# Kernel tuning notes

Measured on AMD Instinct MI355X. Metric: run time of the kernel, lower is better.

## Reference

```python
import jax, jax.numpy as jnp
import numpy as np

N, T, D, H = 2048, 4, 64, 4  # nodes, time steps, per-head dim (=dim), heads


def setup_inputs() -> dict:
    key = jax.random.key(0)
    ks = jax.random.split(key, 9)
    x = jax.random.normal(ks[0], (N, T, D), dtype=jnp.float32)
    Wq = jax.random.normal(ks[1], (H * D, D), dtype=jnp.float32) * 0.05
    bq = jnp.zeros((H * D,), dtype=jnp.float32)
    Wk = jax.random.normal(ks[2], (H * D, D), dtype=jnp.float32) * 0.05
    bk = jnp.zeros((H * D,), dtype=jnp.float32)
    Wv = jax.random.normal(ks[3], (H * D, D), dtype=jnp.float32) * 0.05
    bv = jnp.zeros((H * D,), dtype=jnp.float32)
    attention_weights = jax.random.uniform(ks[4], (T, H, N, N), dtype=jnp.float32)
    attention_mask = jax.random.bernoulli(ks[5], 0.1, (T, H, N, N))
    return {"x": x, "Wq": Wq, "bq": bq, "Wk": Wk, "bk": bk, "Wv": Wv, "bv": bv,
            "attention_weights": attention_weights, "attention_mask": attention_mask}


def reference(x, Wq, bq, Wk, bk, Wv, bv, attention_weights, attention_mask):
    n, t, d = x.shape
    h = Wq.shape[0] // d

    def proj(W, b):
        # (N,T,H*D) -> (N,T,H,D) -> (T,H,N,D)
        return (x @ W.T + b).reshape(n, t, h, d).transpose(1, 2, 0, 3)

    q = proj(Wq, bq)
    k = proj(Wk, bk)
    v = proj(Wv, bv)

    scores = jnp.einsum('thnd,thmd->thnm', q, k) / (d ** 0.5)  # (T,H,N,N)

    raw_att = jax.nn.softmax(scores, axis=-1)
    # torch permutes (T,H,N,D)->(H,N,T,D) contiguous then views as (N,T,H*D);
    # reproduce that exact memory reinterpretation.
    out_raw = jnp.einsum('thnm,thmd->thnd', raw_att, v).transpose(1, 2, 0, 3).reshape(n, t, h * d)

    att = scores * attention_weights
    att = jnp.where(attention_mask, -jnp.inf, att)
    att = jax.nn.softmax(att, axis=-1)
    out = jnp.einsum('thnm,thmd->thnd', att, v).transpose(1, 2, 0, 3).reshape(n, t, h * d)

    return (out, out_raw, raw_att[-1, 0, :, :])
```

## Files before the change

kernel.cpp:

```cpp
#include <hip/hip_runtime.h>
#include <hip/hip_bf16.h>

typedef __attribute__((ext_vector_type(8))) short short8;
typedef __attribute__((ext_vector_type(4))) float float4v;
typedef __attribute__((ext_vector_type(4))) int   int4v;

constexpr int NN = 2048;
constexpr int TT = 4;
constexpr int HH = 4;
constexpr int DD = 64;
constexpr int THC = TT * HH;
constexpr int NTILE = NN / 64;

__device__ __forceinline__ float bf2f(unsigned short u) {
    union { unsigned int i; float f; } c; c.i = ((unsigned int)u) << 16; return c.f;
}
__device__ __forceinline__ unsigned short f2bf(float f) {
    union { float f; unsigned int i; } c; c.f = f;
    unsigned int x = c.i;
    x += 0x7FFFu + ((x >> 16) & 1u);
    return (unsigned short)(x >> 16);
}

__device__ __forceinline__ int mask_code_of(const unsigned int* mw) {
    int okInt = 1, okF32 = 1, okB = 1, anyLow = 0;
    for (int i = 0; i < 256; i++) {
        unsigned int w = mw[i];
        if (w > 1u) okInt = 0;
        if (!(w == 0u || w == 0x3F800000u)) okF32 = 0;
        unsigned int lo = w & 0xFFFFu, hi = w >> 16;
        if (!((lo == 0u || lo == 0x3F80u) && (hi == 0u || hi == 0x3F80u))) okB = 0;
        if (lo == 0x3F80u) anyLow = 1;
    }
    if (okInt) return 1;
    if (okF32 && !anyLow) return 2;
    if (okB) return 3;
    return 0;
}

__device__ __forceinline__ void load_mask_raw(const void* p, size_t idx, int code,
                                              int4v mr[4]) {
    if (code == 1) {
        const int4v* mp = (const int4v*)((const int*)p + idx);
        #pragma unroll
        for (int q = 0; q < 4; q++) mr[q] = mp[q];
    } else if (code == 2) {
        const int4v* mp = (const int4v*)((const float*)p + idx);
        #pragma unroll
        for (int q = 0; q < 4; q++) mr[q] = mp[q];
    } else if (code == 3) {
        const int4v* mp = (const int4v*)((const unsigned short*)p + idx);
        mr[0] = mp[0]; mr[1] = mp[1];
    } else {
        mr[0] = *(const int4v*)((const unsigned char*)p + idx);
    }
}
__device__ __forceinline__ unsigned decode_pm(const int4v mr[4], int code) {
    unsigned pm = 0u;
    if (code == 1) {
        #pragma unroll
        for (int q = 0; q < 4; q++)
            #pragma unroll
            for (int e = 0; e < 4; e++)
                if (mr[q][e] != 0) pm |= 1u << (q * 4 + e);
    } else if (code == 2) {
        #pragma unroll
        for (int q = 0; q < 4; q++)
            #pragma unroll
            for (int e = 0; e < 4; e++)
                if ((((unsigned)mr[q][e]) << 1) != 0u) pm |= 1u << (q * 4 + e);
    } else if (code == 3) {
        #pragma unroll
        for (int q = 0; q < 2; q++)
            #pragma unroll
            for (int e = 0; e < 4; e++) {
                unsigned w = (unsigned)mr[q][e];
                if (w & 0xFFFFu) pm |= 1u << (q * 8 + e * 2);
                if (w >> 16)     pm |= 1u << (q * 8 + e * 2 + 1);
            }
    } else {
        #pragma unroll
        for (int q = 0; q < 4; q++) {
            unsigned w = (unsigned)mr[0][q];
            #pragma unroll
            for (int b = 0; b < 4; b++)
                if ((w >> (8 * b)) & 0xFFu) pm |= 1u << (q * 4 + b);
        }
    }
    return pm;
}

constexpr int PROJ_ROWS = 8;
__global__ __launch_bounds__(256) void proj_b16v_kernel(
    const float* __restrict__ x,
    const float* __restrict__ Wq, const float* __restrict__ bq,
    const float* __restrict__ Wk, const float* __restrict__ bk,
    const float* __restrict__ Wv, const float* __restrict__ bv,
    unsigned short* __restrict__ q16, unsigned short* __restrict__ k16,
    unsigned short* __restrict__ v16)
{
    __shared__ float xl[PROJ_ROWS][64];
    const int tid = threadIdx.x;
    const int r0 = blockIdx.x * PROJ_ROWS;
    for (int i = tid; i < PROJ_ROWS * 64; i += 256)
        xl[i >> 6][i & 63] = x[(size_t)r0 * 64 + i];
    __syncthreads();

    const int c = tid;
    const int hh = c >> 6, dd = c & 63;
    const float* Ws[3] = { Wq, Wk, Wv };
    const float* bs[3] = { bq, bk, bv };
    unsigned short* os[3] = { q16, k16, v16 };

    #pragma unroll
    for (int m = 0; m < 3; m++) {
        float4v wr4[16];
        #pragma unroll
        for (int i = 0; i < 16; i++)
            wr4[i] = *(const float4v*)&Ws[m][(size_t)c * 64 + i * 4];
        const float bias = bs[m][c];
        #pragma unroll
        for (int rr = 0; rr < PROJ_ROWS; rr++) {
            float a = bias;
            #pragma unroll
            for (int i = 0; i < 16; i++) {
                a = fmaf(wr4[i][0], xl[rr][4*i+0], a);
                a = fmaf(wr4[i][1], xl[rr][4*i+1], a);
                a = fmaf(wr4[i][2], xl[rr][4*i+2], a);
                a = fmaf(wr4[i][3], xl[rr][4*i+3], a);
            }
            if (m == 0) a *= 0.125f;
            const int r = r0 + rr;
            const int n = r >> 2, t = r & 3;
            const int th = t * HH + hh;
            os[m][((size_t)th * NN + n) * DD + dd] = f2bf(a);
        }
    }
}

__global__ __launch_bounds__(128, 2) void attn_mfma3_kernel(
    const unsigned short* __restrict__ q16, const unsigned short* __restrict__ k16,
    const unsigned short* __restrict__ v16,
    const float* __restrict__ watt, const void* __restrict__ maskp,
    float* __restrict__ out, float* __restrict__ out_raw)
{
    const int code = mask_code_of((const unsigned int*)maskp);
    const int tid  = threadIdx.x;
    const int wv   = tid >> 6;
    const int lane = tid & 63;
    const int g    = lane >> 4;
    const int j0   = lane & 15;
    const int lr   = lane >> 2;
    const int lc   = lane & 3;

    const int gid = blockIdx.x;
    const int th  = ((gid & 7) << 1) | ((gid >> 3) & 1);
    const int bx  = gid >> 4;
    const int t = th >> 2, h = th & 3;
    const int row0 = bx * 32 + wv * 16;

    const unsigned short* Qb = q16 + (size_t)th * NN * DD;
    const unsigned short* Kb = k16 + (size_t)th * NN * DD;
    const unsigned short* Vb = v16 + (size_t)th * NN * DD;

    __shared__ unsigned short Kl[64][80];
    __shared__ unsigned short Vt[64][80];
    __shared__ float          Sl[2][16][68];
    __shared__ unsigned short Pl[2][16][80];

    short8 aq0, aq1;
    {
        const unsigned short* qp = Qb + (size_t)(row0 + j0) * DD + g * 8;
        aq0 = *(const short8*)qp;
        aq1 = *(const short8*)(qp + 32);
    }

    float m_r = -1e30f, l_r = 0.f, m_w = -1e30f, l_w = 0.f;
    float4v o_r[4], o_w[4];
    #pragma unroll
    for (int ns = 0; ns < 4; ns++) {
        o_r[ns] = (float4v){0.f, 0.f, 0.f, 0.f};
        o_w[ns] = (float4v){0.f, 0.f, 0.f, 0.f};
    }

    const size_t mrow = ((size_t)th * NN + row0 + lr) * NN;

    const int kr = tid >> 1;
    const int kc = (tid & 1) << 5;
    const unsigned short* Kp = Kb + (size_t)kr * DD + kc;
    const unsigned short* Vp = Vb + (size_t)kr * DD + kc;

    short8  kreg[4], vreg[4];
    float4v wcur[4], wnxt[4];
    int4v   mnxt[4];
    unsigned pm;

    #pragma unroll
    for (int u = 0; u < 4; u++) {
        kreg[u] = ((const short8*)Kp)[u];
        vreg[u] = ((const short8*)Vp)[u];
    }
    {
        const float* wp = watt + mrow + lc * 16;
        #pragma unroll
        for (int q = 0; q < 4; q++) wcur[q] = *(const float4v*)&wp[q * 4];
    }
    load_mask_raw(maskp, mrow + lc * 16, code, mnxt);
    #pragma unroll
    for (int u = 0; u < 4; u++) {
        *(short8*)&Kl[kr][kc + u * 8] = kreg[u];
        #pragma unroll
        for (int e = 0; e < 8; e++)
            Vt[kc + u * 8 + e][kr] = (unsigned short)vreg[u][e];
    }
    __syncthreads();
    pm = decode_pm(mnxt, code);

    for (int it = 0; it < NTILE; ++it) {
        if (it + 1 < NTILE) {
            const size_t kvn = (size_t)(it + 1) * 64;
            const unsigned short* kp = Kp + kvn * DD;
            const unsigned short* vp = Vp + kvn * DD;
            #pragma unroll
            for (int u = 0; u < 4; u++) {
                kreg[u] = ((const short8*)kp)[u];
                vreg[u] = ((const short8*)vp)[u];
            }
            const float* wp = watt + mrow + kvn + lc * 16;
            #pragma unroll
            for (int q = 0; q < 4; q++) wnxt[q] = *(const float4v*)&wp[q * 4];
            load_mask_raw(maskp, mrow + kvn + lc * 16, code, mnxt);
        }

        float4v acc[4];
        #pragma unroll
        for (int c = 0; c < 4; c++) {
            short8 b0 = *(const short8*)&Kl[c * 16 + j0][g * 8];
            short8 b1 = *(const short8*)&Kl[c * 16 + j0][32 + g * 8];
            float4v z = (float4v){0.f, 0.f, 0.f, 0.f};
            z = __builtin_amdgcn_mfma_f32_16x16x32_bf16(aq0, b0, z, 0, 0, 0);
            z = __builtin_amdgcn_mfma_f32_16x16x32_bf16(aq1, b1, z, 0, 0, 0);
            acc[c] = z;
        }
        #pragma unroll
        for (int c = 0; c < 4; c++)
            #pragma unroll
            for (int i = 0; i < 4; i++)
                Sl[wv][g * 4 + i][c * 16 + j0] = acc[c][i];
        float4v s4[4];
        #pragma unroll
        for (int q = 0; q < 4; q++)
            s4[q] = *(const float4v*)&Sl[wv][lr][lc * 16 + q * 4];

        {
            float tmax = -3.0e38f;
            #pragma unroll
            for (int q = 0; q < 4; q++)
                #pragma unroll
                for (int e = 0; e < 4; e++) tmax = fmaxf(tmax, s4[q][e]);
            tmax = fmaxf(tmax, __shfl_xor(tmax, 1, 64));
            tmax = fmaxf(tmax, __shfl_xor(tmax, 2, 64));
            float mn = fmaxf(m_r, tmax);
            float alpha = __expf(m_r - mn);
            m_r = mn;
            alignas(16) unsigned short pb[16];
            float tsum = 0.f;
            #pragma unroll
            for (int q = 0; q < 4; q++)
                #pragma unroll
                for (int e = 0; e < 4; e++) {
                    unsigned short b = f2bf(__expf(s4[q][e] - mn));
                    pb[q * 4 + e] = b; tsum += bf2f(b);
                }
            tsum += __shfl_xor(tsum, 1, 64);
            tsum += __shfl_xor(tsum, 2, 64);
            l_r = l_r * alpha + tsum;
            *(short8*)&Pl[wv][lr][lc * 16]     = *(const short8*)&pb[0];
            *(short8*)&Pl[wv][lr][lc * 16 + 8] = *(const short8*)&pb[8];
            float aR[4];
            #pragma unroll
            for (int i = 0; i < 4; i++) aR[i] = __shfl(alpha, (g * 4 + i) * 4, 64);
            #pragma unroll
            for (int ns = 0; ns < 4; ns++)
                #pragma unroll
                for (int i = 0; i < 4; i++) o_r[ns][i] *= aR[i];
            #pragma unroll
            for (int ks2 = 0; ks2 < 2; ks2++) {
                short8 pa = *(const short8*)&Pl[wv][j0][ks2 * 32 + g * 8];
                #pragma unroll
                for (int ns = 0; ns < 4; ns++) {
                    short8 vb8 = *(const short8*)&Vt[ns * 16 + j0][ks2 * 32 + g * 8];
                    o_r[ns] = __builtin_amdgcn_mfma_f32_16x16x32_bf16(pa, vb8, o_r[ns], 0, 0, 0);
                }
            }
        }

        {
            float sw[16];
            #pragma unroll
            for (int q = 0; q < 4; q++)
                #pragma unroll
                for (int e = 0; e < 4; e++) {
                    const int k = q * 4 + e;
                    sw[k] = ((pm >> k) & 1u) ? -1e30f : s4[q][e] * wcur[q][e];
                }
            float tmax = -3.0e38f;
            #pragma unroll
            for (int k = 0; k < 16; k++) tmax = fmaxf(tmax, sw[k]);
            tmax = fmaxf(tmax, __shfl_xor(tmax, 1, 64));
            tmax = fmaxf(tmax, __shfl_xor(tmax, 2, 64));
            float mn = fmaxf(m_w, tmax);
            float alpha = __expf(m_w - mn);
            m_w = mn;
            alignas(16) unsigned short pb[16];
            float tsum = 0.f;
            #pragma unroll
            for (int k = 0; k < 16; k++) {
                unsigned short b = f2bf(__expf(sw[k] - mn));
                pb[k] = b; tsum += bf2f(b);
            }
            tsum += __shfl_xor(tsum, 1, 64);
            tsum += __shfl_xor(tsum, 2, 64);
            l_w = l_w * alpha + tsum;
            *(short8*)&Pl[wv][lr][lc * 16]     = *(const short8*)&pb[0];
            *(short8*)&Pl[wv][lr][lc * 16 + 8] = *(const short8*)&pb[8];
            float aW[4];
            #pragma unroll
            for (int i = 0; i < 4; i++) aW[i] = __shfl(alpha, (g * 4 + i) * 4, 64);
            #pragma unroll
            for (int ns = 0; ns < 4; ns++)
                #pragma unroll
                for (int i = 0; i < 4; i++) o_w[ns][i] *= aW[i];
            #pragma unroll
            for (int ks2 = 0; ks2 < 2; ks2++) {
                short8 pa = *(const short8*)&Pl[wv][j0][ks2 * 32 + g * 8];
                #pragma unroll
                for (int ns = 0; ns < 4; ns++) {
                    short8 vb8 = *(const short8*)&Vt[ns * 16 + j0][ks2 * 32 + g * 8];
                    o_w[ns] = __builtin_amdgcn_mfma_f32_16x16x32_bf16(pa, vb8, o_w[ns], 0, 0, 0);
                }
            }
        }

        __syncthreads();
        if (it + 1 < NTILE) {
            #pragma unroll
            for (int u = 0; u < 4; u++) {
                *(short8*)&Kl[kr][kc + u * 8] = kreg[u];
                #pragma unroll
                for (int e = 0; e < 8; e++)
                    Vt[kc + u * 8 + e][kr] = (unsigned short)vreg[u][e];
            }
            #pragma unroll
            for (int q = 0; q < 4; q++) wcur[q] = wnxt[q];
            pm = decode_pm(mnxt, code);
        }
        __syncthreads();
    }

    float lR[4], lW[4];
    #pragma unroll
    for (int i = 0; i < 4; i++) {
        lR[i] = __shfl(l_r, (g * 4 + i) * 4, 64);
        lW[i] = __shfl(l_w, (g * 4 + i) * 4, 64);
    }
    #pragma unroll
    for (int i = 0; i < 4; i++) {
        const int row = row0 + g * 4 + i;
        const size_t ob = (((size_t)h * NN + row) * TT + t) * DD;
        const float ir = 1.0f / lR[i];
        const float iw = 1.0f / lW[i];
        #pragma unroll
        for (int ns = 0; ns < 4; ns++) {
            out[ob + ns * 16 + j0]     = o_w[ns][i] * iw;
            out_raw[ob + ns * 16 + j0] = o_r[ns][i] * ir;
        }
    }
}

__global__ __launch_bounds__(256) void slice_b16_kernel(
    const unsigned short* __restrict__ q16, const unsigned short* __restrict__ k16,
    float* __restrict__ out_sl)
{
    const int tid = threadIdx.x;
    const int w = tid >> 6, lane = tid & 63;
    const int thsel = 12;
    const unsigned short* Kb = k16 + (size_t)thsel * NN * DD;

    __shared__ float Tt[64][65];
    __shared__ float sr[4][NN];
    __shared__ float ql[4][64];

    ql[tid >> 6][tid & 63] =
        bf2f(q16[((size_t)thsel * NN + blockIdx.x * 4 + (tid >> 6))* DD + (tid & 63)]);
    __syncthreads();
    float qr[64];
    #pragma unroll
    for (int d = 0; d < 64; d++) qr[d] = ql[w][d];

    for (int kt = 0; kt < NN / 64; ++kt) {
        __syncthreads();
        const unsigned short* Ks = Kb + (size_t)kt * 64 * DD;
        #pragma unroll
        for (int u = 0; u < 16; ++u) {
            int e = u * 256 + tid;
            Tt[e >> 6][e & 63] = bf2f(Ks[e]);
        }
        __syncthreads();
        float a = 0.f;
        #pragma unroll
        for (int d = 0; d < 64; ++d)
            a = fmaf(qr[d], Tt[lane][d], a);
        sr[w][kt * 64 + lane] = a;
    }

    const int r = blockIdx.x * 4 + w;
    float mx = -3.0e38f;
    for (int m = lane; m < NN; m += 64) mx = fmaxf(mx, sr[w][m]);
    #pragma unroll
    for (int o = 1; o < 64; o <<= 1) mx = fmaxf(mx, __shfl_xor(mx, o, 64));
    float se = 0.f;
    for (int m = lane; m < NN; m += 64) se += __expf(sr[w][m] - mx);
    #pragma unroll
    for (int o = 1; o < 64; o <<= 1) se += __shfl_xor(se, o, 64);
    const float inv = 1.0f / se;
    for (int m = lane; m < NN; m += 64)
        out_sl[(size_t)r * NN + m] = __expf(sr[w][m] - mx) * inv;
}

extern "C" void kernel_launch(void* const* d_in, const int* in_sizes, int n_in,
                              void* d_out, int out_size, void* d_ws, size_t ws_size,
                              hipStream_t stream)
{
    (void)in_sizes; (void)n_in; (void)out_size; (void)ws_size;
    const float* x    = (const float*)d_in[0];
    const float* Wq   = (const float*)d_in[1];
    const float* bq   = (const float*)d_in[2];
    const float* Wk   = (const float*)d_in[3];
    const float* bk   = (const float*)d_in[4];
    const float* Wv   = (const float*)d_in[5];
    const float* bv   = (const float*)d_in[6];
    const float* watt = (const float*)d_in[7];
    const void*  mask = d_in[8];

    unsigned short* q16 = (unsigned short*)d_ws;
    unsigned short* k16 = q16 + (size_t)THC * NN * DD;
    unsigned short* v16 = k16 + (size_t)THC * NN * DD;

    float* out     = (float*)d_out;
    float* out_raw = out + (size_t)NN * TT * HH * DD;
    float* out_sl  = out + 2 * (size_t)NN * TT * HH * DD;

    proj_b16v_kernel<<<NN * TT / PROJ_ROWS, 256, 0, stream>>>(
        x, Wq, bq, Wk, bk, Wv, bv, q16, k16, v16);
    attn_mfma3_kernel<<<(NN / 32) * THC, 128, 0, stream>>>(
        q16, k16, v16, watt, mask, out, out_raw);
    slice_b16_kernel<<<NN / 4, 256, 0, stream>>>(q16, k16, out_sl);
}
```

Baseline: 295.5 us.

## Pre-transpose V and read K/V directly from global in single-wave attention blocks

Adds a separate kernel that transposes V into a d-major layout, stored temporarily in the slice output buffer, so the attention kernel can load V fragments straight from global memory. The attention kernel drops the shared K/V staging and the block barriers, becomes one wave per block handling 16 rows, and reads K directly from global. The two P·V MFMA passes are merged so each V fragment feeds both accumulators. This removes LDS transposes and synchronisation, but every wave now re-reads K/V from cache instead of sharing them through LDS, and weight/mask prefetching is no longer double-buffered.

```diff
diff --git a/kernel.cpp b/kernel.cpp
--- a/kernel.cpp
+++ b/kernel.cpp
@@ -10,7 +10,6 @@
 constexpr int HH = 4;
 constexpr int DD = 64;
 constexpr int THC = TT * HH;
-constexpr int NTILE = NN / 64;
 
 __device__ __forceinline__ float bf2f(unsigned short u) {
     union { unsigned int i; float f; } c; c.i = ((unsigned int)u) << 16; return c.f;
@@ -138,35 +137,62 @@
     }
 }
 
-__global__ __launch_bounds__(128, 2) void attn_mfma3_kernel(
+__global__ __launch_bounds__(256) void vtrans_kernel(
+    const unsigned short* __restrict__ v16, unsigned short* __restrict__ v16t)
+{
+    __shared__ unsigned int Tl[64][65];
+    const int tid = threadIdx.x;
+    const int th = blockIdx.x >> 5;
+    const int n0 = (blockIdx.x & 31) * 64;
+    const unsigned short* src = v16 + ((size_t)th * NN + n0) * DD;
+    {
+        const int r = tid >> 2, c0 = (tid & 3) * 16;
+        short8 a0 = *(const short8*)&src[(size_t)r * DD + c0];
+        short8 a1 = *(const short8*)&src[(size_t)r * DD + c0 + 8];
+        #pragma unroll
+        for (int e = 0; e < 8; e++) {
+            Tl[r][c0 + e]     = (unsigned short)a0[e];
+            Tl[r][c0 + 8 + e] = (unsigned short)a1[e];
+        }
+    }
+    __syncthreads();
+    {
+        const int dr = tid >> 2, c0 = (tid & 3) * 16;
+        alignas(16) unsigned short tmp[16];
+        #pragma unroll
+        for (int j = 0; j < 16; j++) tmp[j] = (unsigned short)Tl[c0 + j][dr];
+        unsigned short* dst = v16t + ((size_t)th * DD + dr) * NN + n0 + c0;
+        *(short8*)&dst[0] = *(const short8*)&tmp[0];
+        *(short8*)&dst[8] = *(const short8*)&tmp[8];
+    }
+}
+
+__global__ __launch_bounds__(64, 4) void attn_mfma4_kernel(
     const unsigned short* __restrict__ q16, const unsigned short* __restrict__ k16,
-    const unsigned short* __restrict__ v16,
+    const unsigned short* __restrict__ v16t,
     const float* __restrict__ watt, const void* __restrict__ maskp,
     float* __restrict__ out, float* __restrict__ out_raw)
 {
     const int code = mask_code_of((const unsigned int*)maskp);
-    const int tid  = threadIdx.x;
-    const int wv   = tid >> 6;
-    const int lane = tid & 63;
+    const int lane = threadIdx.x;
     const int g    = lane >> 4;
     const int j0   = lane & 15;
     const int lr   = lane >> 2;
     const int lc   = lane & 3;
 
     const int gid = blockIdx.x;
-    const int th  = ((gid & 7) << 1) | ((gid >> 3) & 1);
+    const int th  = gid & 15;
     const int bx  = gid >> 4;
     const int t = th >> 2, h = th & 3;
-    const int row0 = bx * 32 + wv * 16;
-
-    const unsigned short* Qb = q16 + (size_t)th * NN * DD;
-    const unsigned short* Kb = k16 + (size_t)th * NN * DD;
-    const unsigned short* Vb = v16 + (size_t)th * NN * DD;
-
-    __shared__ unsigned short Kl[64][80];
-    __shared__ unsigned short Vt[64][80];
-    __shared__ float          Sl[2][16][68];
-    __shared__ unsigned short Pl[2][16][80];
+    const int row0 = bx * 16;
+
+    const unsigned short* Qb  = q16  + (size_t)th * NN * DD;
+    const unsigned short* Kb  = k16  + (size_t)th * NN * DD;
+    const unsigned short* Vtb = v16t + (size_t)th * DD * NN;
+
+    __shared__ float          Sl[16][68];
+    __shared__ unsigned short PlR[16][72];
+    __shared__ unsigned short PlW[16][72];
 
     short8 aq0, aq1;
     {
@@ -185,58 +211,22 @@
 
     const size_t mrow = ((size_t)th * NN + row0 + lr) * NN;
 
-    const int kr = tid >> 1;
-    const int kc = (tid & 1) << 5;
-    const unsigned short* Kp = Kb + (size_t)kr * DD + kc;
-    const unsigned short* Vp = Vb + (size_t)kr * DD + kc;
-
-    short8  kreg[4], vreg[4];
-    float4v wcur[4], wnxt[4];
-    int4v   mnxt[4];
-    unsigned pm;
-
-    #pragma unroll
-    for (int u = 0; u < 4; u++) {
-        kreg[u] = ((const short8*)Kp)[u];
-        vreg[u] = ((const short8*)Vp)[u];
-    }
-    {
-        const float* wp = watt + mrow + lc * 16;
-        #pragma unroll
-        for (int q = 0; q < 4; q++) wcur[q] = *(const float4v*)&wp[q * 4];
-    }
-    load_mask_raw(maskp, mrow + lc * 16, code, mnxt);
-    #pragma unroll
-    for (int u = 0; u < 4; u++) {
-        *(short8*)&Kl[kr][kc + u * 8] = kreg[u];
-        #pragma unroll
-        for (int e = 0; e < 8; e++)
-            Vt[kc + u * 8 + e][kr] = (unsigned short)vreg[u][e];
-    }
-    __syncthreads();
-    pm = decode_pm(mnxt, code);
-
-    for (int it = 0; it < NTILE; ++it) {
-        if (it + 1 < NTILE) {
-            const size_t kvn = (size_t)(it + 1) * 64;
-            const unsigned short* kp = Kp + kvn * DD;
-            const unsigned short* vp = Vp + kvn * DD;
-            #pragma unroll
-            for (int u = 0; u < 4; u++) {
-                kreg[u] = ((const short8*)kp)[u];
-                vreg[u] = ((const short8*)vp)[u];
-            }
-            const float* wp = watt + mrow + kvn + lc * 16;
-            #pragma unroll
-            for (int q = 0; q < 4; q++) wnxt[q] = *(const float4v*)&wp[q * 4];
-            load_mask_raw(maskp, mrow + kvn + lc * 16, code, mnxt);
+    for (int kv0 = 0; kv0 < NN; kv0 += 64) {
+        float4v wv4[4];
+        int4v   mk4[4];
+        {
+            const float* wp = watt + mrow + kv0 + lc * 16;
+            #pragma unroll
+            for (int q = 0; q < 4; q++) wv4[q] = *(const float4v*)&wp[q * 4];
+            load_mask_raw(maskp, mrow + kv0 + lc * 16, code, mk4);
         }
 
         float4v acc[4];
         #pragma unroll
         for (int c = 0; c < 4; c++) {
-            short8 b0 = *(const short8*)&Kl[c * 16 + j0][g * 8];
-            short8 b1 = *(const short8*)&Kl[c * 16 + j0][32 + g * 8];
+            const unsigned short* kp = Kb + (size_t)(kv0 + c * 16 + j0) * DD + g * 8;
+            short8 b0 = *(const short8*)kp;
+            short8 b1 = *(const short8*)(kp + 32);
             float4v z = (float4v){0.f, 0.f, 0.f, 0.f};
             z = __builtin_amdgcn_mfma_f32_16x16x32_bf16(aq0, b0, z, 0, 0, 0);
             z = __builtin_amdgcn_mfma_f32_16x16x32_bf16(aq1, b1, z, 0, 0, 0);
@@ -246,11 +236,11 @@
         for (int c = 0; c < 4; c++)
             #pragma unroll
             for (int i = 0; i < 4; i++)
-                Sl[wv][g * 4 + i][c * 16 + j0] = acc[c][i];
+                Sl[g * 4 + i][c * 16 + j0] = acc[c][i];
         float4v s4[4];
         #pragma unroll
         for (int q = 0; q < 4; q++)
-            s4[q] = *(const float4v*)&Sl[wv][lr][lc * 16 + q * 4];
+            s4[q] = *(const float4v*)&Sl[lr][lc * 16 + q * 4];
 
         {
             float tmax = -3.0e38f;
@@ -275,8 +265,8 @@
             tsum += __shfl_xor(tsum, 1, 64);
             tsum += __shfl_xor(tsum, 2, 64);
             l_r = l_r * alpha + tsum;
-            *(short8*)&Pl[wv][lr][lc * 16]     = *(const short8*)&pb[0];
-            *(short8*)&Pl[wv][lr][lc * 16 + 8] = *(const short8*)&pb[8];
+            *(short8*)&PlR[lr][lc * 16]     = *(const short8*)&pb[0];
+            *(short8*)&PlR[lr][lc * 16 + 8] = *(const short8*)&pb[8];
             float aR[4];
             #pragma unroll
             for (int i = 0; i < 4; i++) aR[i] = __shfl(alpha, (g * 4 + i) * 4, 64);
@@ -284,25 +274,17 @@
             for (int ns = 0; ns < 4; ns++)
                 #pragma unroll
                 for (int i = 0; i < 4; i++) o_r[ns][i] *= aR[i];
-            #pragma unroll
-            for (int ks2 = 0; ks2 < 2; ks2++) {
-                short8 pa = *(const short8*)&Pl[wv][j0][ks2 * 32 + g * 8];
-                #pragma unroll
-                for (int ns = 0; ns < 4; ns++) {
-                    short8 vb8 = *(const short8*)&Vt[ns * 16 + j0][ks2 * 32 + g * 8];
-                    o_r[ns] = __builtin_amdgcn_mfma_f32_16x16x32_bf16(pa, vb8, o_r[ns], 0, 0, 0);
-                }
-            }
         }
 
         {
+            const unsigned pm = decode_pm(mk4, code);
             float sw[16];
             #pragma unroll
             for (int q = 0; q < 4; q++)
                 #pragma unroll
                 for (int e = 0; e < 4; e++) {
                     const int k = q * 4 + e;
-                    sw[k] = ((pm >> k) & 1u) ? -1e30f : s4[q][e] * wcur[q][e];
+                    sw[k] = ((pm >> k) & 1u) ? -1e30f : s4[q][e] * wv4[q][e];
                 }
             float tmax = -3.0e38f;
             #pragma unroll
@@ -322,8 +304,8 @@
             tsum += __shfl_xor(tsum, 1, 64);
             tsum += __shfl_xor(tsum, 2, 64);
             l_w = l_w * alpha + tsum;
-            *(short8*)&Pl[wv][lr][lc * 16]     = *(const short8*)&pb[0];
-            *(short8*)&Pl[wv][lr][lc * 16 + 8] = *(const short8*)&pb[8];
+            *(short8*)&PlW[lr][lc * 16]     = *(const short8*)&pb[0];
+            *(short8*)&PlW[lr][lc * 16 + 8] = *(const short8*)&pb[8];
             float aW[4];
             #pragma unroll
             for (int i = 0; i < 4; i++) aW[i] = __shfl(alpha, (g * 4 + i) * 4, 64);
@@ -331,31 +313,21 @@
             for (int ns = 0; ns < 4; ns++)
                 #pragma unroll
                 for (int i = 0; i < 4; i++) o_w[ns][i] *= aW[i];
-            #pragma unroll
-            for (int ks2 = 0; ks2 < 2; ks2++) {
-                short8 pa = *(const short8*)&Pl[wv][j0][ks2 * 32 + g * 8];
-                #pragma unroll
-                for (int ns = 0; ns < 4; ns++) {
-                    short8 vb8 = *(const short8*)&Vt[ns * 16 + j0][ks2 * 32 + g * 8];
-                    o_w[ns] = __builtin_amdgcn_mfma_f32_16x16x32_bf16(pa, vb8, o_w[ns], 0, 0, 0);
-                }
+        }
+
+        #pragma unroll
+        for (int ks2 = 0; ks2 < 2; ks2++) {
+            short8 paR = *(const short8*)&PlR[j0][ks2 * 32 + g * 8];
+            short8 paW = *(const short8*)&PlW[j0][ks2 * 32 + g * 8];
+            #pragma unroll
+            for (int ns = 0; ns < 4; ns++) {
+                const unsigned short* vp =
+                    Vtb + (size_t)(ns * 16 + j0) * NN + kv0 + ks2 * 32 + g * 8;
+                short8 vb8 = *(const short8*)vp;
+                o_r[ns] = __builtin_amdgcn_mfma_f32_16x16x32_bf16(paR, vb8, o_r[ns], 0, 0, 0);
+                o_w[ns] = __builtin_amdgcn_mfma_f32_16x16x32_bf16(paW, vb8, o_w[ns], 0, 0, 0);
             }
         }
-
-        __syncthreads();
-        if (it + 1 < NTILE) {
-            #pragma unroll
-            for (int u = 0; u < 4; u++) {
-                *(short8*)&Kl[kr][kc + u * 8] = kreg[u];
-                #pragma unroll
-                for (int e = 0; e < 8; e++)
-                    Vt[kc + u * 8 + e][kr] = (unsigned short)vreg[u][e];
-            }
-            #pragma unroll
-            for (int q = 0; q < 4; q++) wcur[q] = wnxt[q];
-            pm = decode_pm(mnxt, code);
-        }
-        __syncthreads();
     }
 
     float lR[4], lW[4];
@@ -451,9 +423,12 @@
     float* out_raw = out + (size_t)NN * TT * HH * DD;
     float* out_sl  = out + 2 * (size_t)NN * TT * HH * DD;
 
+    unsigned short* v16t = (unsigned short*)out_sl;
+
     proj_b16v_kernel<<<NN * TT / PROJ_ROWS, 256, 0, stream>>>(
         x, Wq, bq, Wk, bk, Wv, bv, q16, k16, v16);
-    attn_mfma3_kernel<<<(NN / 32) * THC, 128, 0, stream>>>(
-        q16, k16, v16, watt, mask, out, out_raw);
+    vtrans_kernel<<<THC * (NN / 64), 256, 0, stream>>>(v16, v16t);
+    attn_mfma4_kernel<<<(NN / 16) * THC, 64, 0, stream>>>(
+        q16, k16, v16t, watt, mask, out, out_raw);
     slice_b16_kernel<<<NN / 4, 256, 0, stream>>>(q16, k16, out_sl);
 }
```

Measured after the change: 395.4 us. 1.34x slower.
